# Optimization experiments

Hardware: AMD Instinct MI355X
Metric: run time of the kernel (lower is better)

## Reference

```python
import jax, jax.numpy as jnp
import numpy as np

D_MODEL = 1024
NUM_HEADS = 16
HEAD_DIM = D_MODEL // NUM_HEADS
THETA = 10000.0
B, S = 2, 2048


def _apply_rope(t, cos, sin):
    # t: [B, H, S, hd]; cos/sin: [S, hd//2]
    te = t[..., 0::2]
    to = t[..., 1::2]
    re = te * cos - to * sin
    ro = te * sin + to * cos
    out = jnp.stack([re, ro], axis=-1)  # [B,H,S,hd//2,2]
    return out.reshape(t.shape)


def setup_inputs() -> dict:
    key = jax.random.key(0)
    kx, kq, kk, kv, ko = jax.random.split(key, 5)
    std = 2.0 / (2 * D_MODEL) ** 0.5
    def w(k):
        return jnp.clip(std * jax.random.normal(k, (D_MODEL, D_MODEL), jnp.float32), -3.0 * std, 3.0 * std)
    return {
        "x": jax.random.normal(kx, (B, S, D_MODEL), jnp.float32),
        "Wq": w(kq),
        "Wk": w(kk),
        "Wv": w(kv),
        "Wo": w(ko),
    }


def reference(x, Wq, Wk, Wv, Wo):
    Bv, Sv, _ = x.shape
    def proj(W):
        return jnp.einsum('bsd,ed->bse', x, W).reshape(Bv, Sv, NUM_HEADS, HEAD_DIM).transpose(0, 2, 1, 3)
    q, k, v = proj(Wq), proj(Wk), proj(Wv)

    pos = jnp.arange(Sv, dtype=jnp.float32)
    inv_freq = THETA ** (-jnp.arange(0, HEAD_DIM, 2, dtype=jnp.float32) / HEAD_DIM)
    ang = pos[:, None] * inv_freq[None, :]  # [S, hd//2]
    cos, sin = jnp.cos(ang), jnp.sin(ang)
    q = _apply_rope(q, cos, sin)
    k = _apply_rope(k, cos, sin)

    scale = 1.0 / jnp.sqrt(jnp.float32(HEAD_DIM))
    scores = jnp.einsum('bhqd,bhkd->bhqk', q.astype(jnp.float32), k.astype(jnp.float32)) * scale
    causal = jnp.tril(jnp.ones((Sv, Sv), dtype=bool))
    scores = jnp.where(causal[None, None], scores, -jnp.inf)
    attn = jax.nn.softmax(scores, axis=-1)
    out = jnp.einsum('bhqk,bhkd->bhqd', attn, v.astype(jnp.float32))
    out = out.transpose(0, 2, 1, 3).reshape(Bv, Sv, D_MODEL)
    return jnp.einsum('bsd,ed->bse', out, Wo)
```

## Files before the change

### kernel.cpp

```cpp
#include <hip/hip_runtime.h>
#include <hip/hip_bf16.h>
#include <stdint.h>

typedef __bf16 bf16x8 __attribute__((ext_vector_type(8)));
typedef float  f32x4  __attribute__((ext_vector_type(4)));

__device__ __forceinline__ float bf2f(unsigned short u) {
    union { float f; uint32_t i; } v; v.i = ((uint32_t)u) << 16; return v.f;
}
__device__ __forceinline__ unsigned short f2bf(float f) {
    union { float f; uint32_t i; } v; v.f = f;
    uint32_t r = v.i + 0x7FFF + ((v.i >> 16) & 1);
    return (unsigned short)(r >> 16);
}
__device__ __forceinline__ unsigned short f2bf_rz(float f) {
    union { float f; uint32_t i; } v; v.f = f;
    return (unsigned short)(v.i >> 16);
}

#define GLD_LDS(gptr, lptr) \
    __builtin_amdgcn_global_load_lds( \
        (const __attribute__((address_space(1))) void*)(gptr), \
        (__attribute__((address_space(3))) void*)(lptr), 16, 0, 0)

__global__ __launch_bounds__(256) void convert_inputs(
    const void* __restrict__ x,  const void* __restrict__ wq,
    const void* __restrict__ wk, const void* __restrict__ wv,
    const void* __restrict__ wo, unsigned short* __restrict__ dst,
    unsigned short* __restrict__ wob_dst, int* __restrict__ flag)
{
    __shared__ int cnt[256];
    const int tid = threadIdx.x;
    uint32_t u = ((const uint32_t*)x)[tid];
    int e = (u >> 7) & 0xFF;
    cnt[tid] = (e >= 100 && e <= 140) ? 1 : 0;
    __syncthreads();
    for (int s = 128; s > 0; s >>= 1) {
        if (tid < s) cnt[tid] += cnt[tid + s];
        __syncthreads();
    }
    const int isf32 = (cnt[0] >= 128) ? 0 : 1;
    if (blockIdx.x == 0 && tid == 0) flag[0] = isf32 ? 0 : 1;

    int c = blockIdx.x * 256 + tid;
    const void* src; size_t off; unsigned short* out;
    if (c < 524288)      { src = x;  off = (size_t)c * 8;            out = dst + (size_t)c * 8; }
    else if (c < 655360) { src = wq; off = (size_t)(c - 524288) * 8; out = dst + (size_t)c * 8; }
    else if (c < 786432) { src = wk; off = (size_t)(c - 655360) * 8; out = dst + (size_t)c * 8; }
    else if (c < 917504) { src = wv; off = (size_t)(c - 786432) * 8; out = dst + (size_t)c * 8; }
    else                 { src = wo; off = (size_t)(c - 917504) * 8; out = wob_dst + off; }
    unsigned short t[8];
    if (isf32) {
        const float* s = (const float*)src + off;
        float4 f0 = *(const float4*)s;
        float4 f1 = *(const float4*)(s + 4);
        t[0] = f2bf(f0.x); t[1] = f2bf(f0.y); t[2] = f2bf(f0.z); t[3] = f2bf(f0.w);
        t[4] = f2bf(f1.x); t[5] = f2bf(f1.y); t[6] = f2bf(f1.z); t[7] = f2bf(f1.w);
    } else {
        *(uint4*)t = *(const uint4*)((const unsigned short*)src + off);
    }
    *(uint4*)out = *(const uint4*)t;
}

__global__ __launch_bounds__(256) void gemm_bt(
    const unsigned short* __restrict__ A,
    const unsigned short* __restrict__ B0,
    const unsigned short* __restrict__ B1,
    const unsigned short* __restrict__ B2,
    unsigned short* __restrict__ O0,
    unsigned short* __restrict__ O1,
    unsigned short* __restrict__ O2)
{
    const int K = 1024;
    __shared__ __align__(16) unsigned short As[64 * 64];
    __shared__ __align__(16) unsigned short Bs[128 * 64];

    const int tid  = threadIdx.x;
    const int lane = tid & 63;
    const int wid  = tid >> 6;
    const int wm   = wid >> 1;
    const int wn   = wid & 1;
    const int lr   = lane & 15;
    const int quad = lane >> 4;
    const int q8   = quad * 8;

    const int m0  = blockIdx.y * 64;
    const int n0g = blockIdx.x * 128;
    const int sel = n0g >> 10;
    const unsigned short* B = (sel == 0) ? B0 : ((sel == 1) ? B1 : B2);
    unsigned short* Optr    = (sel == 0) ? O0 : ((sel == 1) ? O1 : O2);
    const int n0  = n0g & 1023;

    f32x4 acc[2][4] = {};

    for (int kk = 0; kk < K; kk += 64) {
        __syncthreads();
        for (int p = 0; p < 2; ++p) {
            int c   = p * 256 + tid;
            int row = c >> 3;
            int c8  = (c & 7) * 8;
            GLD_LDS(&A[(size_t)(m0 + row) * K + kk + c8], &As[c * 8]);
        }
        for (int p = 0; p < 4; ++p) {
            int c   = p * 256 + tid;
            int row = c >> 3;
            int c8  = (c & 7) * 8;
            GLD_LDS(&B[(size_t)(n0 + row) * K + kk + c8], &Bs[c * 8]);
        }
        __syncthreads();

        for (int ks = 0; ks < 64; ks += 32) {
            bf16x8 af[2], bf[4];
            for (int t = 0; t < 2; ++t)
                af[t] = *(const bf16x8*)&As[(wm * 32 + t * 16 + lr) * 64 + ks + q8];
            for (int t = 0; t < 4; ++t)
                bf[t] = *(const bf16x8*)&Bs[(wn * 64 + t * 16 + lr) * 64 + ks + q8];
            for (int mt = 0; mt < 2; ++mt)
                for (int nt = 0; nt < 4; ++nt)
                    acc[mt][nt] = __builtin_amdgcn_mfma_f32_16x16x32_bf16(
                        af[mt], bf[nt], acc[mt][nt], 0, 0, 0);
        }
    }

    for (int mt = 0; mt < 2; ++mt) {
        for (int nt = 0; nt < 4; ++nt) {
            for (int r = 0; r < 4; ++r) {
                int m  = m0 + wm * 32 + mt * 16 + quad * 4 + r;
                int nl = n0 + wn * 64 + nt * 16 + lr;
                int b = m >> 11, s = m & 2047;
                int h = nl >> 6, d = nl & 63;
                Optr[((size_t)(b * 16 + h) * 2048 + s) * 64 + d] = f2bf(acc[mt][nt][r]);
            }
        }
    }
}

__global__ __launch_bounds__(256) void gemm_out(
    const unsigned short* __restrict__ P0,
    const unsigned short* __restrict__ P1,
    const float* __restrict__ Lsum,
    const unsigned short* __restrict__ B0,
    void* __restrict__ O,
    const int* __restrict__ flag)
{
    const int K = 1024;
    __shared__ __align__(16) unsigned short As[64 * 64];
    __shared__ __align__(16) unsigned short Bs[128 * 64];

    const int isf32 = (flag[0] == 0) ? 1 : 0;

    const int tid  = threadIdx.x;
    const int lane = tid & 63;
    const int wid  = tid >> 6;
    const int wm   = wid >> 1;
    const int wn   = wid & 1;
    const int lr   = lane & 15;
    const int quad = lane >> 4;
    const int q8   = quad * 8;

    const int m0 = blockIdx.y * 64;
    const int n0 = blockIdx.x * 128;

    f32x4 acc[2][4] = {};

    for (int kk = 0; kk < K; kk += 64) {
        __syncthreads();
        const int h = kk >> 6;
        for (int p = 0; p < 2; ++p) {
            int c   = p * 256 + tid;
            int row = c >> 3;
            int d0  = (c & 7) * 8;
            int m   = m0 + row;
            int b   = m >> 11, s = m & 2047;
            int li  = (b * 16 + h) * 2048 + s;
            float inv = 1.0f / (Lsum[li] + Lsum[65536 + li]);
            size_t addr = ((size_t)li) * 64 + d0;
            unsigned short a[8], bb[8], o[8];
            *(uint4*)a  = *(const uint4*)&P0[addr];
            *(uint4*)bb = *(const uint4*)&P1[addr];
            for (int j = 0; j < 8; ++j)
                o[j] = f2bf((bf2f(a[j]) + bf2f(bb[j])) * inv);
            *(uint4*)&As[c * 8] = *(const uint4*)o;
        }
        for (int p = 0; p < 4; ++p) {
            int c   = p * 256 + tid;
            int row = c >> 3;
            int c8  = (c & 7) * 8;
            GLD_LDS(&B0[(size_t)(n0 + row) * K + kk + c8], &Bs[c * 8]);
        }
        __syncthreads();

        for (int ks = 0; ks < 64; ks += 32) {
            bf16x8 af[2], bf[4];
            for (int t = 0; t < 2; ++t)
                af[t] = *(const bf16x8*)&As[(wm * 32 + t * 16 + lr) * 64 + ks + q8];
            for (int t = 0; t < 4; ++t)
                bf[t] = *(const bf16x8*)&Bs[(wn * 64 + t * 16 + lr) * 64 + ks + q8];
            for (int mt = 0; mt < 2; ++mt)
                for (int nt = 0; nt < 4; ++nt)
                    acc[mt][nt] = __builtin_amdgcn_mfma_f32_16x16x32_bf16(
                        af[mt], bf[nt], acc[mt][nt], 0, 0, 0);
        }
    }

    for (int mt = 0; mt < 2; ++mt) {
        for (int nt = 0; nt < 4; ++nt) {
            for (int r = 0; r < 4; ++r) {
                int m  = m0 + wm * 32 + mt * 16 + quad * 4 + r;
                int nl = n0 + wn * 64 + nt * 16 + lr;
                float val = acc[mt][nt][r];
                if (isf32) ((float*)O)[(size_t)m * 1024 + nl] = val;
                else ((unsigned short*)O)[(size_t)m * 1024 + nl] = f2bf(val);
            }
        }
    }
}

__global__ __launch_bounds__(256) void rope_transpose(
    unsigned short* __restrict__ Q, unsigned short* __restrict__ Kp,
    const unsigned short* __restrict__ V, unsigned short* __restrict__ Vt)
{
    __shared__ unsigned short T[64 * 65];
    const int tid = threadIdx.x;

    if (blockIdx.x < 4096) {
        const int CH = 32 * 2048 * 8;
        int idx = blockIdx.x * 256 + tid;
        bool isK = idx >= CH;
        int j = isK ? (idx - CH) : idx;
        unsigned short* p = isK ? Kp : Q;

        int c8   = j & 7;
        int srow = j >> 3;
        int s    = srow & 2047;
        int off  = srow * 64 + c8 * 8;

        uint4 raw = *(const uint4*)&p[off];
        unsigned short t[8];
        *(uint4*)t = raw;
        float sf = (float)s;
        float qs = isK ? 1.0f : 0.125f;
        for (int jj = 0; jj < 4; ++jj) {
            int i = c8 * 4 + jj;
            float inv = __expf(-0.2878231366f * (float)i);
            float ang = sf * inv;
            float sn = __sinf(ang);
            float cs = __cosf(ang);
            float e = bf2f(t[2 * jj]);
            float o = bf2f(t[2 * jj + 1]);
            t[2 * jj]     = f2bf((e * cs - o * sn) * qs);
            t[2 * jj + 1] = f2bf((e * sn + o * cs) * qs);
        }
        *(uint4*)&p[off] = *(const uint4*)t;
    } else {
        int bidx = blockIdx.x - 4096;
        const int s0 = (bidx & 31) * 64;
        const int bh = bidx >> 5;

        const unsigned short* src = V + ((size_t)bh * 2048 + s0) * 64;
        for (int p = 0; p < 2; ++p) {
            int c = p * 256 + tid;
            int s  = c >> 3;
            int d8 = (c & 7) * 8;
            uint4 raw = *(const uint4*)&src[s * 64 + d8];
            unsigned short t[8];
            *(uint4*)t = raw;
            for (int j = 0; j < 8; ++j) T[s * 65 + d8 + j] = t[j];
        }
        __syncthreads();
        unsigned short* dst = Vt + (size_t)bh * 64 * 2048 + s0;
        for (int p = 0; p < 2; ++p) {
            int c = p * 256 + tid;
            int d  = c >> 3;
            int s8 = (c & 7) * 8;
            unsigned short t[8];
            for (int j = 0; j < 8; ++j) t[j] = T[(s8 + j) * 65 + d];
            *(uint4*)&dst[(size_t)d * 2048 + s8] = *(const uint4*)t;
        }
    }
}

__global__ __launch_bounds__(256) void attn_kernel(
    const unsigned short* __restrict__ Q,
    const unsigned short* __restrict__ Kp,
    const unsigned short* __restrict__ Vt,
    unsigned short* __restrict__ P0,
    unsigned short* __restrict__ P1,
    float* __restrict__ Lsum)
{
    __shared__ __align__(16) unsigned short Ks[2][4096];
    __shared__ __align__(16) unsigned short Vs[2][4096];
    __shared__ __align__(16) unsigned short Ps[4096];

    const int tid  = threadIdx.x;
    const int lane = tid & 63;
    const int w    = tid >> 6;
    const int lr   = lane & 15;
    const int quad = lane >> 4;
    const int q8   = quad * 8;
    const int wps  = w * 1024;

    const int bh    = blockIdx.x;
    const int y     = blockIdx.y;
    const int split = y >> 4;
    const int yq    = y & 15;
    const int qb    = (yq < 8) ? yq : (23 - yq);
    const int q0    = qb * 128;
    const int kb0   = split ? (qb + 1) : 0;
    const int kb1   = split ? (2 * qb + 1) : qb;

    unsigned short* Pout = split ? P1 : P0;

    const unsigned short* KbBase = Kp + (size_t)bh * 2048 * 64;
    const unsigned short* VbBase = Vt + (size_t)bh * 131072;

    auto stage = [&](int kb, int buf) {
        const unsigned short* Kb = KbBase + kb * 64 * 64;
        const unsigned short* Vb = VbBase + kb * 64;
        for (int p = 0; p < 2; ++p) {
            int c    = p * 256 + tid;
            int f    = c >> 6, l = c & 63;
            int nt   = f >> 1, ks = f & 1;
            int lr_s = l & 15, qd = l >> 4;
            GLD_LDS(&Kb[(nt * 16 + lr_s) * 64 + ks * 32 + qd * 8], &Ks[buf][c * 8]);
            GLD_LDS(&Vb[(size_t)(nt * 16 + lr_s) * 2048 + ks * 32 + qd * 8], &Vs[buf][c * 8]);
        }
    };

    bf16x8 qa[2][2];
    for (int mt = 0; mt < 2; ++mt) {
        const unsigned short* Qw = Q + ((size_t)bh * 2048 + q0 + mt * 64 + w * 16 + lr) * 64;
        qa[mt][0] = *(const bf16x8*)&Qw[q8];
        qa[mt][1] = *(const bf16x8*)&Qw[32 + q8];
    }

    stage(kb0, 0);

    f32x4 oacc[2][4] = {};
    float lpart[2][4] = {};
    const int l8 = lane * 8;
    const int lr7 = lr & 7;
    const int lrh = lr >> 3;

    for (int kb = kb0; kb <= kb1; ++kb) {
        const int cur = (kb - kb0) & 1;
        __syncthreads();
        if (kb < kb1) stage(kb + 1, cur ^ 1);

        f32x4 sacc[2][4] = {};
        for (int nt = 0; nt < 4; ++nt) {
            bf16x8 kf0 = *(const bf16x8*)&Ks[cur][(nt * 2 + 0) * 512 + l8];
            bf16x8 kf1 = *(const bf16x8*)&Ks[cur][(nt * 2 + 1) * 512 + l8];
            for (int mt = 0; mt < 2; ++mt) {
                sacc[mt][nt] = __builtin_amdgcn_mfma_f32_16x16x32_bf16(qa[mt][0], kf0, sacc[mt][nt], 0, 0, 0);
                sacc[mt][nt] = __builtin_amdgcn_mfma_f32_16x16x32_bf16(qa[mt][1], kf1, sacc[mt][nt], 0, 0, 0);
            }
        }

        if (kb >= 2 * qb) {
            for (int mt = 0; mt < 2; ++mt) {
                int rowb = q0 + mt * 64 + w * 16 + quad * 4;
                for (int nt = 0; nt < 4; ++nt) {
                    int col = kb * 64 + nt * 16 + lr;
                    for (int r = 0; r < 4; ++r)
                        if (col > rowb + r) sacc[mt][nt][r] = -3.0e38f;
                }
            }
        }

        for (int mt = 0; mt < 2; ++mt) {
            for (int r = 0; r < 4; ++r) {
                for (int nt = 0; nt < 4; ++nt) {
                    float pv = __expf(sacc[mt][nt][r] - 16.0f);
                    lpart[mt][r] += pv;
                    int ks = nt >> 1;
                    int qr = (nt * 2 + lrh) & 3;
                    Ps[wps + ks * 512 + (qr * 16 + quad * 4 + r) * 8 + lr7] = f2bf_rz(pv);
                }
            }
            for (int ks = 0; ks < 2; ++ks) {
                bf16x8 pa = *(const bf16x8*)&Ps[wps + ks * 512 + l8];
                for (int nt = 0; nt < 4; ++nt) {
                    bf16x8 vf = *(const bf16x8*)&Vs[cur][(nt * 2 + ks) * 512 + l8];
                    oacc[mt][nt] = __builtin_amdgcn_mfma_f32_16x16x32_bf16(pa, vf, oacc[mt][nt], 0, 0, 0);
                }
            }
        }
    }

    for (int mt = 0; mt < 2; ++mt) {
        for (int r = 0; r < 4; ++r) {
            float l = lpart[mt][r];
            for (int off = 1; off < 16; off <<= 1)
                l += __shfl_xor(l, off, 64);
            int s = q0 + mt * 64 + w * 16 + quad * 4 + r;
            for (int nt = 0; nt < 4; ++nt)
                Pout[((size_t)bh * 2048 + s) * 64 + nt * 16 + lr] = f2bf_rz(oacc[mt][nt][r]);
            if (lr == 0) Lsum[split * 65536 + bh * 2048 + s] = l;
        }
    }
}

extern "C" void kernel_launch(void* const* d_in, const int* in_sizes, int n_in,
                              void* d_out, int out_size, void* d_ws, size_t ws_size,
                              hipStream_t stream)
{
    const void* x  = d_in[0];
    const void* Wq = d_in[1];
    const void* Wk = d_in[2];
    const void* Wv = d_in[3];
    const void* Wo = d_in[4];

    int* flag = (int*)d_ws;
    unsigned short* base = (unsigned short*)d_ws + 8;
    const size_t M1 = 1048576;
    unsigned short* xb  = base;
    unsigned short* wqb = base + 4 * M1;
    unsigned short* wkb = base + 5 * M1;
    unsigned short* wvb = base + 6 * M1;
    unsigned short* q   = base + 8 * M1;
    unsigned short* k   = base + 12 * M1;
    unsigned short* v   = base + 16 * M1;
    unsigned short* wob = base + 20 * M1;
    float*          Ls  = (float*)(base + 21 * M1);
    unsigned short* vt  = xb;
    unsigned short* P0  = v;
    unsigned short* P1  = wqb;

    convert_inputs<<<dim3(4096), 256, 0, stream>>>(x, Wq, Wk, Wv, Wo, base, wob, flag);
    gemm_bt<<<dim3(24, 64), 256, 0, stream>>>(xb, wqb, wkb, wvb, q, k, v);
    rope_transpose<<<dim3(5120), 256, 0, stream>>>(q, k, v, vt);
    attn_kernel<<<dim3(32, 32), 256, 0, stream>>>(q, k, vt, P0, P1, Ls);
    gemm_out<<<dim3(8, 64), 256, 0, stream>>>(P0, P1, Ls, wob, d_out, flag);
}
```

Baseline: 225.0 us.

## Rewrite QKV projection GEMM as 256x256-tile double-buffered 8-phase pipelined kernel

Replaces the 64x128-tile, 256-thread QKV GEMM with a 256x256-tile, 512-thread kernel that double-buffers A and B tiles in LDS with XOR-swizzled layout. Global-to-LDS loads for later k-tiles are interleaved with four MFMA quadrant phases per iteration, using explicit vmcnt/lgkmcnt waits, barriers and setprio. The aim is to raise operand reuse, avoid LDS bank conflicts and overlap memory with compute. The cost is heavy LDS use (128KB) and only 192 blocks, which is fewer than two waves across the CUs and risks imbalance.

```diff
diff --git a/kernel.cpp b/kernel.cpp
--- a/kernel.cpp
+++ b/kernel.cpp
@@ -62,7 +62,7 @@
     *(uint4*)out = *(const uint4*)t;
 }
 
-__global__ __launch_bounds__(256) void gemm_bt(
+__global__ __launch_bounds__(512, 2) void gemm_qkv_8ph(
     const unsigned short* __restrict__ A,
     const unsigned short* __restrict__ B0,
     const unsigned short* __restrict__ B1,
@@ -71,68 +71,162 @@
     unsigned short* __restrict__ O1,
     unsigned short* __restrict__ O2)
 {
-    const int K = 1024;
-    __shared__ __align__(16) unsigned short As[64 * 64];
-    __shared__ __align__(16) unsigned short Bs[128 * 64];
+    __shared__ __align__(16) unsigned short Asl[2][16384];
+    __shared__ __align__(16) unsigned short Bsl[2][16384];
 
     const int tid  = threadIdx.x;
     const int lane = tid & 63;
     const int wid  = tid >> 6;
-    const int wm   = wid >> 1;
-    const int wn   = wid & 1;
+    const int wm   = wid >> 2;
+    const int wn   = wid & 3;
     const int lr   = lane & 15;
     const int quad = lane >> 4;
-    const int q8   = quad * 8;
-
-    const int m0  = blockIdx.y * 64;
-    const int n0g = blockIdx.x * 128;
+
+    const int m0  = blockIdx.y * 256;
+    const int n0g = blockIdx.x * 256;
     const int sel = n0g >> 10;
-    const unsigned short* B = (sel == 0) ? B0 : ((sel == 1) ? B1 : B2);
-    unsigned short* Optr    = (sel == 0) ? O0 : ((sel == 1) ? O1 : O2);
+    const unsigned short* Bp = (sel == 0) ? B0 : ((sel == 1) ? B1 : B2);
+    unsigned short* Optr     = (sel == 0) ? O0 : ((sel == 1) ? O1 : O2);
     const int n0  = n0g & 1023;
 
-    f32x4 acc[2][4] = {};
-
-    for (int kk = 0; kk < K; kk += 64) {
-        __syncthreads();
-        for (int p = 0; p < 2; ++p) {
-            int c   = p * 256 + tid;
-            int row = c >> 3;
-            int c8  = (c & 7) * 8;
-            GLD_LDS(&A[(size_t)(m0 + row) * K + kk + c8], &As[c * 8]);
-        }
-        for (int p = 0; p < 4; ++p) {
-            int c   = p * 256 + tid;
-            int row = c >> 3;
-            int c8  = (c & 7) * 8;
-            GLD_LDS(&B[(size_t)(n0 + row) * K + kk + c8], &Bs[c * 8]);
-        }
-        __syncthreads();
-
-        for (int ks = 0; ks < 64; ks += 32) {
-            bf16x8 af[2], bf[4];
-            for (int t = 0; t < 2; ++t)
-                af[t] = *(const bf16x8*)&As[(wm * 32 + t * 16 + lr) * 64 + ks + q8];
-            for (int t = 0; t < 4; ++t)
-                bf[t] = *(const bf16x8*)&Bs[(wn * 64 + t * 16 + lr) * 64 + ks + q8];
-            for (int mt = 0; mt < 2; ++mt)
-                for (int nt = 0; nt < 4; ++nt)
-                    acc[mt][nt] = __builtin_amdgcn_mfma_f32_16x16x32_bf16(
-                        af[mt], bf[nt], acc[mt][nt], 0, 0, 0);
-        }
-    }
-
-    for (int mt = 0; mt < 2; ++mt) {
-        for (int nt = 0; nt < 4; ++nt) {
-            for (int r = 0; r < 4; ++r) {
-                int m  = m0 + wm * 32 + mt * 16 + quad * 4 + r;
-                int nl = n0 + wn * 64 + nt * 16 + lr;
-                int b = m >> 11, s = m & 2047;
-                int h = nl >> 6, d = nl & 63;
-                Optr[((size_t)(b * 16 + h) * 2048 + s) * 64 + d] = f2bf(acc[mt][nt][r]);
+    const int sw0 = ((0 + quad) ^ (lr & 7)) * 8;
+    const int sw1 = ((4 + quad) ^ (lr & 7)) * 8;
+
+    f32x4 acc[2][4][2][2] = {};
+    bf16x8 aF[4][2];
+    bf16x8 bF[2][2];
+
+#define STAGEA(T, H) do { \
+    const int tA_ = (T); \
+    _Pragma("unroll") \
+    for (int p_ = 0; p_ < 2; ++p_) { \
+        int c_   = p_ * 512 + tid; \
+        int row_ = c_ >> 3; \
+        int sc_  = ((c_ & 7) ^ (row_ & 7)) * 8; \
+        GLD_LDS(&A[(size_t)(m0 + (H) * 128 + row_) * 1024 + tA_ * 64 + sc_], \
+                &Asl[tA_ & 1][(H) * 8192 + c_ * 8]); \
+    } } while (0)
+
+#define STAGEB(T, H) do { \
+    const int tB_ = (T); \
+    _Pragma("unroll") \
+    for (int p_ = 0; p_ < 2; ++p_) { \
+        int c_   = p_ * 512 + tid; \
+        int row_ = c_ >> 3; \
+        int sc_  = ((c_ & 7) ^ (row_ & 7)) * 8; \
+        GLD_LDS(&Bp[(size_t)(n0 + (H) * 128 + row_) * 1024 + tB_ * 64 + sc_], \
+                &Bsl[tB_ & 1][(H) * 8192 + c_ * 8]); \
+    } } while (0)
+
+#define LOADA(BUF, QM) do { \
+    _Pragma("unroll") \
+    for (int fm_ = 0; fm_ < 4; ++fm_) { \
+        const int row_ = (QM) * 128 + wm * 64 + fm_ * 16 + lr; \
+        aF[fm_][0] = *(const bf16x8*)&Asl[BUF][row_ * 64 + sw0]; \
+        aF[fm_][1] = *(const bf16x8*)&Asl[BUF][row_ * 64 + sw1]; \
+    } } while (0)
+
+#define LOADB(BUF, QN) do { \
+    _Pragma("unroll") \
+    for (int fn_ = 0; fn_ < 2; ++fn_) { \
+        const int row_ = (QN) * 128 + wn * 32 + fn_ * 16 + lr; \
+        bF[fn_][0] = *(const bf16x8*)&Bsl[BUF][row_ * 64 + sw0]; \
+        bF[fn_][1] = *(const bf16x8*)&Bsl[BUF][row_ * 64 + sw1]; \
+    } } while (0)
+
+#define MFMA16(QM, QN) do { \
+    __builtin_amdgcn_s_setprio(1); \
+    _Pragma("unroll") \
+    for (int fm_ = 0; fm_ < 4; ++fm_) { \
+        _Pragma("unroll") \
+        for (int fn_ = 0; fn_ < 2; ++fn_) { \
+            acc[QM][fm_][QN][fn_] = __builtin_amdgcn_mfma_f32_16x16x32_bf16( \
+                aF[fm_][0], bF[fn_][0], acc[QM][fm_][QN][fn_], 0, 0, 0); \
+            acc[QM][fm_][QN][fn_] = __builtin_amdgcn_mfma_f32_16x16x32_bf16( \
+                aF[fm_][1], bF[fn_][1], acc[QM][fm_][QN][fn_], 0, 0, 0); \
+        } \
+    } \
+    __builtin_amdgcn_s_setprio(0); \
+    } while (0)
+
+#define BARRIER() __builtin_amdgcn_s_barrier()
+#define LGKM0()   asm volatile("s_waitcnt lgkmcnt(0)" ::: "memory")
+
+    STAGEB(0, 0);
+    STAGEA(0, 1);
+    STAGEA(0, 0);
+    STAGEB(0, 1);
+    STAGEB(1, 0);
+    STAGEA(1, 1);
+    asm volatile("s_waitcnt vmcnt(4)" ::: "memory");
+    BARRIER();
+
+    const int NT = 16;
+#pragma unroll 2
+    for (int t = 0; t < NT; ++t) {
+        const int buf = t & 1;
+
+        LOADA(buf, 0);
+        LOADB(buf, 0);
+        if (t + 1 < NT) STAGEA(t + 1, 0);
+        BARRIER();
+        LGKM0();
+        MFMA16(0, 0);
+        BARRIER();
+
+        LOADA(buf, 1);
+        if (t + 1 < NT) STAGEB(t + 1, 1);
+        BARRIER();
+        LGKM0();
+        MFMA16(1, 0);
+        BARRIER();
+
+        LOADB(buf, 1);
+        if (t + 2 < NT) STAGEB(t + 2, 0);
+        BARRIER();
+        LGKM0();
+        MFMA16(1, 1);
+        BARRIER();
+
+        LOADA(buf, 0);
+        if (t + 2 < NT) STAGEA(t + 2, 1);
+        BARRIER();
+        LGKM0();
+        MFMA16(0, 1);
+        if (t + 2 < NT) asm volatile("s_waitcnt vmcnt(4)" ::: "memory");
+        else            asm volatile("s_waitcnt vmcnt(0)" ::: "memory");
+        BARRIER();
+    }
+
+#pragma unroll
+    for (int qm = 0; qm < 2; ++qm) {
+#pragma unroll
+        for (int fm = 0; fm < 4; ++fm) {
+            const int mb = m0 + qm * 128 + wm * 64 + fm * 16 + quad * 4;
+#pragma unroll
+            for (int qn = 0; qn < 2; ++qn) {
+#pragma unroll
+                for (int fn = 0; fn < 2; ++fn) {
+                    const int nl = n0 + qn * 128 + wn * 32 + fn * 16 + lr;
+                    const int h = nl >> 6, d = nl & 63;
+#pragma unroll
+                    for (int r = 0; r < 4; ++r) {
+                        const int m = mb + r;
+                        const int b = m >> 11, s = m & 2047;
+                        Optr[((size_t)(b * 16 + h) * 2048 + s) * 64 + d] =
+                            f2bf(acc[qm][fm][qn][fn][r]);
+                    }
+                }
             }
         }
     }
+#undef STAGEA
+#undef STAGEB
+#undef LOADA
+#undef LOADB
+#undef MFMA16
+#undef BARRIER
+#undef LGKM0
 }
 
 __global__ __launch_bounds__(256) void gemm_out(
@@ -428,7 +522,7 @@
     unsigned short* P1  = wqb;
 
     convert_inputs<<<dim3(4096), 256, 0, stream>>>(x, Wq, Wk, Wv, Wo, base, wob, flag);
-    gemm_bt<<<dim3(24, 64), 256, 0, stream>>>(xb, wqb, wkb, wvb, q, k, v);
+    gemm_qkv_8ph<<<dim3(12, 16), 512, 0, stream>>>(xb, wqb, wkb, wvb, q, k, v);
     rope_transpose<<<dim3(5120), 256, 0, stream>>>(q, k, v, vt);
     attn_kernel<<<dim3(32, 32), 256, 0, stream>>>(q, k, vt, P0, P1, Ls);
     gemm_out<<<dim3(8, 64), 256, 0, stream>>>(P0, P1, Ls, wob, d_out, flag);
```

Measured after the change: 215.2 us. 1.05x faster.
